# Optimization experiments

Hardware: AMD Instinct MI355X
Metric: run time of the kernel (lower is better)

Reference implementation:

```python
import jax, jax.numpy as jnp
import numpy as np

S, B, D = 2048, 2, 1024
H, DH = 16, 64
DFF = 4096
E, K = 4, 2
SCALE = 1.0 / (DH ** 0.5)


def _ln(x, g, b, eps):
    m = jnp.mean(x, axis=-1, keepdims=True)
    v = jnp.mean((x - m) ** 2, axis=-1, keepdims=True)
    return (x - m) * jax.lax.rsqrt(v + eps) * g + b


def setup_inputs() -> dict:
    key = jax.random.key(0)
    ks = jax.random.split(key, 12)
    s = lambda k, shape, fan: jax.random.normal(k, shape, jnp.float32) * (fan ** -0.5)
    return {
        "hidden_states": jax.random.normal(ks[0], (S, B, D), jnp.float32),
        "ln_in_g": jnp.ones((D,), jnp.float32), "ln_in_b": jnp.zeros((D,), jnp.float32),
        "Wq": s(ks[1], (D, H * DH), D),
        "Wkv": s(ks[2], (D, 2 * H * DH), D),
        "Wo": s(ks[3], (H * DH, D), H * DH),
        "ln_attn_g": jnp.ones((D,), jnp.float32), "ln_attn_b": jnp.zeros((D,), jnp.float32),
        "ln_post_g": jnp.ones((D,), jnp.float32), "ln_post_b": jnp.zeros((D,), jnp.float32),
        "Wg": s(ks[4], (D, E), D),
        "W1": s(ks[5], (E, D, DFF), D), "b1": jnp.zeros((E, DFF), jnp.float32),
        "W2": s(ks[6], (E, DFF, D), DFF), "b2": jnp.zeros((E, D), jnp.float32),
    }


def reference(hidden_states, ln_in_g, ln_in_b, Wq, Wkv, Wo, ln_attn_g, ln_attn_b,
              ln_post_g, ln_post_b, Wg, W1, b1, W2, b2):
    # --- input layernorm (eps=1e-6) ---
    h = _ln(hidden_states, ln_in_g, ln_in_b, 1e-6)  # [S,B,D]

    # --- MultiHeadAttn2 (post-lnorm, no mask, no mems) ---
    q = (h @ Wq).reshape(S, B, H, DH)
    k, v = jnp.split((h @ Wkv).reshape(S, B, H, 2 * DH), 2, axis=-1)
    score = jnp.einsum('ibnd,jbnd->ijbn', q, k) * SCALE      # [S,S,B,H]
    prob = jax.nn.softmax(score, axis=1)
    attn_vec = jnp.einsum('ijbn,jbnd->ibnd', prob, v).reshape(S, B, H * DH)
    attn_out = attn_vec @ Wo
    attention_output = _ln(h + attn_out, ln_attn_g, ln_attn_b, 1e-5)

    # --- residual + post-attention layernorm (eps=1e-6) ---
    layernorm_input = hidden_states + attention_output
    x = _ln(layernorm_input, ln_post_g, ln_post_b, 1e-6)

    # --- top-k MoE (E=4, k=2, no token dropping) ---
    xt = x.reshape(-1, D)                                     # [T,D]
    probs = jax.nn.softmax(xt @ Wg, axis=-1)                  # [T,E]
    topv, topi = jax.lax.top_k(probs, K)                      # [T,K]
    gates = topv / jnp.sum(topv, axis=-1, keepdims=True)
    cw = jnp.zeros_like(probs)
    for kk in range(K):  # small fixed K
        cw = cw + gates[:, kk:kk + 1] * jax.nn.one_hot(topi[:, kk], E, dtype=probs.dtype)
    hmid = jax.nn.gelu(jnp.einsum('td,edf->tef', xt, W1) + b1, approximate=False)
    y = jnp.einsum('tef,efd->ted', hmid, W2) + b2             # [T,E,D]
    moe_out = jnp.einsum('te,ted->td', cw, y).reshape(S, B, D)

    # load-balancing aux loss: E * sum(mean_probs * top1_fraction)
    me = jnp.mean(probs, axis=0)
    ce = jnp.mean(jax.nn.one_hot(topi[:, 0], E, dtype=probs.dtype), axis=0)
    moe_loss = E * jnp.sum(me * ce)

    output = layernorm_input + moe_out
    return output, moe_loss
```

## Files before the change

kernel.cpp:

```cpp
#include <hip/hip_runtime.h>
#include <cmath>

#define S_   2048
#define B_   2
#define D_   1024
#define H_   16
#define DH_  64
#define DFF_ 4096
#define E_   4
#define T_   4096
#define SCALE_ 0.125f

typedef __attribute__((ext_vector_type(8))) short short8;
typedef __attribute__((ext_vector_type(4))) float f32x4;
typedef __attribute__((ext_vector_type(4))) unsigned short u16x4;
typedef __attribute__((ext_vector_type(4))) unsigned int u32x4;

static __device__ __forceinline__ unsigned short f2bf(float f) {
  union { float f; unsigned int u; } v; v.f = f;
  unsigned int r = v.u + 0x7FFFu + ((v.u >> 16) & 1u);
  return (unsigned short)(r >> 16);
}

static __device__ __forceinline__ float bf2f(unsigned short u) {
  union { unsigned int u; float f; } v; v.u = (unsigned int)u << 16;
  return v.f;
}

static __device__ __forceinline__ f32x4 mfma16(short8 a, short8 b, f32x4 c) {
  return __builtin_amdgcn_mfma_f32_16x16x32_bf16(a, b, c, 0, 0, 0);
}

static __device__ __forceinline__ void gll16(const unsigned short* g, unsigned short* l) {
  __builtin_amdgcn_global_load_lds(
      (const __attribute__((address_space(1))) void*)g,
      (__attribute__((address_space(3))) void*)l, 16, 0, 0);
}

static __device__ __forceinline__ float gelu_f(float vv) {
  float u = 0.7978845608f * (vv + 0.044715f * vv * vv * vv);
  u = fminf(fmaxf(u, -9.0f), 9.0f);
  float e2 = __expf(2.0f * u);
  return vv * e2 * (1.0f / (e2 + 1.0f));
}

__global__ void transpose_cvt(const float* __restrict__ in, unsigned short* __restrict__ out,
                              int R, int C) {
  __shared__ float t[64][33];
  size_t boff = (size_t)blockIdx.z * R * C;
  in += boff; out += boff;
  int c0 = blockIdx.x * 32, r0 = blockIdx.y * 64;
  for (int i = threadIdx.y; i < 64; i += 8)
    t[i][threadIdx.x] = in[(size_t)(r0 + i) * C + c0 + threadIdx.x];
  __syncthreads();
  for (int i = threadIdx.y; i < 32; i += 8) {
    float v0 = t[2 * threadIdx.x][i], v1 = t[2 * threadIdx.x + 1][i];
    unsigned int pk = (unsigned int)f2bf(v0) | ((unsigned int)f2bf(v1) << 16);
    *(unsigned int*)(&out[(size_t)(c0 + i) * R + r0 + 2 * threadIdx.x]) = pk;
  }
}

__global__ void transpose_cvt_split(const float* __restrict__ in,
    unsigned short* __restrict__ outh, unsigned short* __restrict__ outl, int R, int C) {
  __shared__ float t[64][33];
  int c0 = blockIdx.x * 32, r0 = blockIdx.y * 64;
  for (int i = threadIdx.y; i < 64; i += 8)
    t[i][threadIdx.x] = in[(size_t)(r0 + i) * C + c0 + threadIdx.x];
  __syncthreads();
  for (int i = threadIdx.y; i < 32; i += 8) {
    float v0 = t[2 * threadIdx.x][i], v1 = t[2 * threadIdx.x + 1][i];
    unsigned short h0 = f2bf(v0), h1 = f2bf(v1);
    unsigned int hp = (unsigned int)h0 | ((unsigned int)h1 << 16);
    unsigned int lp = (unsigned int)f2bf(v0 - bf2f(h0)) |
                      ((unsigned int)f2bf(v1 - bf2f(h1)) << 16);
    size_t o = (size_t)(c0 + i) * R + r0 + 2 * threadIdx.x;
    *(unsigned int*)(&outh[o]) = hp;
    *(unsigned int*)(&outl[o]) = lp;
  }
}

__global__ __launch_bounds__(256) void v_transpose(
    const unsigned short* __restrict__ kvh, const unsigned short* __restrict__ kvl,
    unsigned short* __restrict__ vTh, unsigned short* __restrict__ vTl) {
  __shared__ unsigned short th[64][72], tl[64][72];
  int j0 = blockIdx.x * 64;
  int bh = blockIdx.y;
  int b = bh & 1, n = bh >> 1;
  int tid = threadIdx.x;
  int jr = tid >> 3, dc = (tid & 7) * 8;
  for (int it = 0; it < 2; ++it) {
    int jj = it * 32 + jr;
    size_t src = ((size_t)((j0 + jj) * 2 + b)) * 2048 + n * 128 + 64 + dc;
    *(short8*)(&th[jj][dc]) = *(const short8*)(kvh + src);
    *(short8*)(&tl[jj][dc]) = *(const short8*)(kvl + src);
  }
  __syncthreads();
  int dr = tid >> 3, jc = (tid & 7) * 8;
  for (int it = 0; it < 2; ++it) {
    int d = it * 32 + dr;
    short8 oh, ol;
    for (int u = 0; u < 8; ++u) { oh[u] = th[jc + u][d]; ol[u] = tl[jc + u][d]; }
    size_t dst = ((size_t)((b * 16 + n) * 64 + d)) * 2048 + j0 + jc;
    *(short8*)(vTh + dst) = oh;
    *(short8*)(vTl + dst) = ol;
  }
}

static __device__ __forceinline__ void block_reduce2(float& s, float& s2, float* sh) {
  __syncthreads();
  for (int off = 32; off; off >>= 1) { s += __shfl_down(s, off); s2 += __shfl_down(s2, off); }
  int w = threadIdx.x >> 6;
  if ((threadIdx.x & 63) == 0) { sh[w * 2] = s; sh[w * 2 + 1] = s2; }
  __syncthreads();
  s = sh[0] + sh[2] + sh[4] + sh[6];
  s2 = sh[1] + sh[3] + sh[5] + sh[7];
}

__global__ __launch_bounds__(256) void ln_in_kernel(const float* __restrict__ hid,
    const float* __restrict__ g, const float* __restrict__ b,
    float* __restrict__ h, unsigned short* __restrict__ hbh, unsigned short* __restrict__ hbl) {
  __shared__ float sh[8];
  int t = blockIdx.x, tid = threadIdx.x;
  size_t ro = (size_t)t * D_;
  f32x4 v = ((const f32x4*)(hid + ro))[tid];
  float s = v[0] + v[1] + v[2] + v[3];
  float s2 = v[0]*v[0] + v[1]*v[1] + v[2]*v[2] + v[3]*v[3];
  block_reduce2(s, s2, sh);
  float mean = s * (1.0f / D_);
  float var = s2 * (1.0f / D_) - mean * mean;
  float rstd = rsqrtf(var + 1e-6f);
  f32x4 gv = ((const f32x4*)g)[tid], bv = ((const f32x4*)b)[tid];
  f32x4 y; u16x4 yh, yl;
  for (int c = 0; c < 4; ++c) {
    float z = (v[c] - mean) * rstd * gv[c] + bv[c];
    y[c] = z; yh[c] = f2bf(z); yl[c] = f2bf(z - bf2f(yh[c]));
  }
  ((f32x4*)(h + ro))[tid] = y;
  ((u16x4*)(hbh + ro))[tid] = yh;
  ((u16x4*)(hbl + ro))[tid] = yl;
}

__global__ __launch_bounds__(256) void ln_fused_kernel(
    const float* __restrict__ hid, const float* __restrict__ h, const float* __restrict__ ao,
    const float* __restrict__ ga, const float* __restrict__ ba,
    const float* __restrict__ gp, const float* __restrict__ bp,
    float* __restrict__ out, float* __restrict__ x, unsigned short* __restrict__ xb) {
  __shared__ float sh[8];
  int t = blockIdx.x, tid = threadIdx.x;
  size_t ro = (size_t)t * D_;
  f32x4 hv = ((const f32x4*)(h + ro))[tid];
  f32x4 av = ((const f32x4*)(ao + ro))[tid];
  f32x4 a = hv + av;
  float s = a[0] + a[1] + a[2] + a[3];
  float s2 = a[0]*a[0] + a[1]*a[1] + a[2]*a[2] + a[3]*a[3];
  block_reduce2(s, s2, sh);
  float mean = s * (1.0f / D_);
  float var = s2 * (1.0f / D_) - mean * mean;
  float rstd = rsqrtf(var + 1e-5f);
  f32x4 lg = ((const f32x4*)ga)[tid], lb = ((const f32x4*)ba)[tid];
  f32x4 hidv = ((const f32x4*)(hid + ro))[tid];
  f32x4 li;
  for (int c = 0; c < 4; ++c) li[c] = hidv[c] + (a[c] - mean) * rstd * lg[c] + lb[c];
  ((f32x4*)(out + ro))[tid] = li;
  float s3 = li[0] + li[1] + li[2] + li[3];
  float s4 = li[0]*li[0] + li[1]*li[1] + li[2]*li[2] + li[3]*li[3];
  block_reduce2(s3, s4, sh);
  float mean2 = s3 * (1.0f / D_);
  float var2 = s4 * (1.0f / D_) - mean2 * mean2;
  float rstd2 = rsqrtf(var2 + 1e-6f);
  f32x4 g2 = ((const f32x4*)gp)[tid], b2v = ((const f32x4*)bp)[tid];
  f32x4 xv; u16x4 xbv;
  for (int c = 0; c < 4; ++c) { float z = (li[c] - mean2) * rstd2 * g2[c] + b2v[c]; xv[c] = z; xbv[c] = f2bf(z); }
  ((f32x4*)(x + ro))[tid] = xv;
  ((u16x4*)(xb + ro))[tid] = xbv;
}

__global__ __launch_bounds__(256) void qkv_gemm(
    const unsigned short* __restrict__ Ah, const unsigned short* __restrict__ Al,
    const unsigned short* __restrict__ WqTh, const unsigned short* __restrict__ WqTl,
    const unsigned short* __restrict__ WkvTh, const unsigned short* __restrict__ WkvTl,
    unsigned short* __restrict__ qh, unsigned short* __restrict__ ql,
    unsigned short* __restrict__ kvh, unsigned short* __restrict__ kvl) {
  const int K = 1024;
  int m0 = blockIdx.y * 128, n0g = blockIdx.x * 128;
  const unsigned short *Bh, *Bl;
  unsigned short *Ch, *Cl;
  int NC, n0;
  if (n0g < 1024) { Bh = WqTh; Bl = WqTl; Ch = qh; Cl = ql; NC = 1024; n0 = n0g; }
  else { Bh = WkvTh; Bl = WkvTl; Ch = kvh; Cl = kvl; NC = 2048; n0 = n0g - 1024; }
  __shared__ unsigned short pool2[16384];
  unsigned short* Ash = pool2;
  unsigned short* Asl = pool2 + 4096;
  unsigned short* Bsh = pool2 + 8192;
  unsigned short* Bsl = pool2 + 12288;
  int tid = threadIdx.x;
  int lane = tid & 63, w = tid >> 6;
  int quad = lane >> 4, l15 = lane & 15;
  int wm = (w >> 1) * 64, wn = (w & 1) * 64;
  f32x4 acc[4][4];
  for (int i = 0; i < 4; ++i) for (int j = 0; j < 4; ++j) acc[i][j] = 0;
  int rs0 = w * 32 + (lane >> 2), rs1 = rs0 + 16;
  int cofs = (lane & 3) * 8;
  const unsigned short* gah0 = Ah + (size_t)(m0 + rs0) * K + cofs;
  const unsigned short* gah1 = Ah + (size_t)(m0 + rs1) * K + cofs;
  const unsigned short* gal0 = Al + (size_t)(m0 + rs0) * K + cofs;
  const unsigned short* gal1 = Al + (size_t)(m0 + rs1) * K + cofs;
  const unsigned short* gbh0 = Bh + (size_t)(n0 + rs0) * K + cofs;
  const unsigned short* gbh1 = Bh + (size_t)(n0 + rs1) * K + cofs;
  const unsigned short* gbl0 = Bl + (size_t)(n0 + rs0) * K + cofs;
  const unsigned short* gbl1 = Bl + (size_t)(n0 + rs1) * K + cofs;
  unsigned short* lA0 = &Ash[(w * 2 + 0) * 512];
  unsigned short* lA1 = &Ash[(w * 2 + 1) * 512];
  unsigned short* lAl0 = &Asl[(w * 2 + 0) * 512];
  unsigned short* lAl1 = &Asl[(w * 2 + 1) * 512];
  unsigned short* lB0 = &Bsh[(w * 2 + 0) * 512];
  unsigned short* lB1 = &Bsh[(w * 2 + 1) * 512];
  unsigned short* lBl0 = &Bsl[(w * 2 + 0) * 512];
  unsigned short* lBl1 = &Bsl[(w * 2 + 1) * 512];
  for (int k0 = 0; k0 < K; k0 += 32) {
    __syncthreads();
    gll16(gah0 + k0, lA0); gll16(gah1 + k0, lA1);
    gll16(gal0 + k0, lAl0); gll16(gal1 + k0, lAl1);
    gll16(gbh0 + k0, lB0); gll16(gbh1 + k0, lB1);
    gll16(gbl0 + k0, lBl0); gll16(gbl1 + k0, lBl1);
    __syncthreads();
    short8 afh[4], afl[4], bfh[4], bfl[4];
    for (int i = 0; i < 4; ++i) {
      int o = (wm + i * 16 + l15) * 32 + quad * 8;
      afh[i] = *(const short8*)(&Ash[o]);
      afl[i] = *(const short8*)(&Asl[o]);
    }
    for (int j = 0; j < 4; ++j) {
      int o = (wn + j * 16 + l15) * 32 + quad * 8;
      bfh[j] = *(const short8*)(&Bsh[o]);
      bfl[j] = *(const short8*)(&Bsl[o]);
    }
    for (int i = 0; i < 4; ++i)
      for (int j = 0; j < 4; ++j) {
        f32x4 a = acc[i][j];
        a = mfma16(afh[i], bfl[j], a);
        a = mfma16(afl[i], bfh[j], a);
        a = mfma16(afh[i], bfh[j], a);
        acc[i][j] = a;
      }
  }
  __syncthreads();
  unsigned short* eph = &pool2[w * 1152];
  unsigned short* epl = &pool2[4608 + w * 1152];
  int row16 = lane >> 3, chunk = lane & 7;
  for (int i = 0; i < 4; ++i) {
    for (int j = 0; j < 4; ++j) {
      f32x4 a = acc[i][j];
      int lo = j * 16 + l15;
      for (int r = 0; r < 4; ++r) {
        unsigned short hb = f2bf(a[r]);
        eph[(quad * 4 + r) * 72 + lo] = hb;
        epl[(quad * 4 + r) * 72 + lo] = f2bf(a[r] - bf2f(hb));
      }
    }
    for (int it = 0; it < 2; ++it) {
      int rr = it * 8 + row16;
      size_t go = (size_t)(m0 + wm + i * 16 + rr) * NC + n0 + wn + chunk * 8;
      *(u32x4*)(&Ch[go]) = *(const u32x4*)(&eph[rr * 72 + chunk * 8]);
      *(u32x4*)(&Cl[go]) = *(const u32x4*)(&epl[rr * 72 + chunk * 8]);
    }
    __syncthreads();
  }
}

template<int MT>
__global__ __launch_bounds__(256) void gemm3f(
    const unsigned short* __restrict__ Ah, const unsigned short* __restrict__ Al,
    const unsigned short* __restrict__ Bh, const unsigned short* __restrict__ Bl,
    float* __restrict__ Cf, int N, int K) {
  int m0 = blockIdx.y * MT, n0 = blockIdx.x * 128;
  __shared__ unsigned short pool3[MT * 64 + 8192];
  unsigned short* Ash = pool3;
  unsigned short* Asl = pool3 + MT * 32;
  unsigned short* Bsh = pool3 + MT * 64;
  unsigned short* Bsl = pool3 + MT * 64 + 4096;
  int tid = threadIdx.x;
  int lane = tid & 63, w = tid >> 6;
  int quad = lane >> 4, l15 = lane & 15;
  int wm = (w >> 1) * (MT / 2), wn = (w & 1) * 64;
  constexpr int MI = MT / 32;
  f32x4 acc[MI][4];
  for (int i = 0; i < MI; ++i) for (int j = 0; j < 4; ++j) acc[i][j] = 0;
  constexpr int AI = MT / 64;
  int cofs = (lane & 3) * 8;
  const unsigned short* gah[AI]; const unsigned short* gal[AI];
  unsigned short *lAh[AI], *lAl[AI];
  for (int is = 0; is < AI; ++is) {
    int rs = w * (MT / 4) + is * 16 + (lane >> 2);
    gah[is] = Ah + (size_t)(m0 + rs) * K + cofs;
    gal[is] = Al + (size_t)(m0 + rs) * K + cofs;
    lAh[is] = &Ash[(w * AI + is) * 512];
    lAl[is] = &Asl[(w * AI + is) * 512];
  }
  int rsB0 = w * 32 + (lane >> 2), rsB1 = rsB0 + 16;
  const unsigned short* gbh0 = Bh + (size_t)(n0 + rsB0) * K + cofs;
  const unsigned short* gbh1 = Bh + (size_t)(n0 + rsB1) * K + cofs;
  const unsigned short* gbl0 = Bl + (size_t)(n0 + rsB0) * K + cofs;
  const unsigned short* gbl1 = Bl + (size_t)(n0 + rsB1) * K + cofs;
  unsigned short* lB0 = &Bsh[(w * 2 + 0) * 512];
  unsigned short* lB1 = &Bsh[(w * 2 + 1) * 512];
  unsigned short* lBl0 = &Bsl[(w * 2 + 0) * 512];
  unsigned short* lBl1 = &Bsl[(w * 2 + 1) * 512];
  for (int k0 = 0; k0 < K; k0 += 32) {
    __syncthreads();
    for (int is = 0; is < AI; ++is) { gll16(gah[is] + k0, lAh[is]); gll16(gal[is] + k0, lAl[is]); }
    gll16(gbh0 + k0, lB0); gll16(gbh1 + k0, lB1);
    gll16(gbl0 + k0, lBl0); gll16(gbl1 + k0, lBl1);
    __syncthreads();
    short8 afh[MI], afl[MI], bfh[4], bfl[4];
    for (int i = 0; i < MI; ++i) {
      int o = (wm + i * 16 + l15) * 32 + quad * 8;
      afh[i] = *(const short8*)(&Ash[o]);
      afl[i] = *(const short8*)(&Asl[o]);
    }
    for (int j = 0; j < 4; ++j) {
      int o = (wn + j * 16 + l15) * 32 + quad * 8;
      bfh[j] = *(const short8*)(&Bsh[o]);
      bfl[j] = *(const short8*)(&Bsl[o]);
    }
    for (int i = 0; i < MI; ++i)
      for (int j = 0; j < 4; ++j) {
        f32x4 a = acc[i][j];
        a = mfma16(afh[i], bfl[j], a);
        a = mfma16(afl[i], bfh[j], a);
        a = mfma16(afh[i], bfh[j], a);
        acc[i][j] = a;
      }
  }
  __syncthreads();
  float* epf = (float*)(pool3 + w * 2176);
  for (int i = 0; i < MI; ++i) {
    for (int j = 0; j < 4; ++j) {
      f32x4 a = acc[i][j];
      for (int r = 0; r < 4; ++r) epf[(quad * 4 + r) * 68 + j * 16 + l15] = a[r];
    }
    for (int it = 0; it < 4; ++it) {
      int rr = (lane >> 4) + it * 4;
      int ch = lane & 15;
      *(f32x4*)(&Cf[(size_t)(m0 + wm + i * 16 + rr) * N + n0 + wn + ch * 4]) =
          *(const f32x4*)(&epf[rr * 68 + ch * 4]);
    }
    __syncthreads();
  }
}

__global__ __launch_bounds__(256) void moe_up(
    const unsigned short* __restrict__ A, const unsigned short* __restrict__ W1T,
    unsigned short* __restrict__ hmid, int N, int K,
    const int* __restrict__ cnt, const int* __restrict__ offs,
    const int* __restrict__ list, const float* __restrict__ b1) {
  int e = blockIdx.y >> 5, mt = blockIdx.y & 31;
  int M = cnt[e];
  int m0 = mt * 128, n0 = blockIdx.x * 128;
  if (M == 0 || m0 >= M) return;
  const unsigned short* Bt = W1T + (size_t)e * DFF_ * D_;
  const int* liste = list + e * T_;
  const float* bias = b1 + (size_t)e * DFF_;
  size_t obase = (size_t)offs[e];
  __shared__ unsigned short pool[16384];
  unsigned short* As0 = pool;
  unsigned short* Bs0 = pool + 4096;
  unsigned short* As1 = pool + 8192;
  unsigned short* Bs1 = pool + 12288;
  int tid = threadIdx.x;
  int lane = tid & 63, w = tid >> 6;
  int quad = lane >> 4, l15 = lane & 15;
  int wm = (w >> 1) * 64, wn = (w & 1) * 64;
  f32x4 acc[4][4];
  for (int i = 0; i < 4; ++i) for (int j = 0; j < 4; ++j) acc[i][j] = 0;
  int rs0 = w * 32 + (lane >> 2), rs1 = rs0 + 16;
  int cofs = (lane & 3) * 8;
  const unsigned short* ga0 = A + (size_t)liste[min(m0 + rs0, M - 1)] * K + cofs;
  const unsigned short* ga1 = A + (size_t)liste[min(m0 + rs1, M - 1)] * K + cofs;
  const unsigned short* gb0 = Bt + (size_t)(n0 + rs0) * K + cofs;
  const unsigned short* gb1 = Bt + (size_t)(n0 + rs1) * K + cofs;
  int so0 = (w * 2 + 0) * 512, so1 = (w * 2 + 1) * 512;
  auto stage = [&](unsigned short* Ab, unsigned short* Bb, int k) {
    gll16(ga0 + k, Ab + so0); gll16(ga1 + k, Ab + so1);
    gll16(gb0 + k, Bb + so0); gll16(gb1 + k, Bb + so1);
  };
  auto compute = [&](const unsigned short* Ab, const unsigned short* Bb) {
    short8 af[4], bfr[4];
    for (int i = 0; i < 4; ++i) af[i] = *(const short8*)(&Ab[(wm + i * 16 + l15) * 32 + quad * 8]);
    for (int j = 0; j < 4; ++j) bfr[j] = *(const short8*)(&Bb[(wn + j * 16 + l15) * 32 + quad * 8]);
    for (int i = 0; i < 4; ++i)
      for (int j = 0; j < 4; ++j)
        acc[i][j] = mfma16(af[i], bfr[j], acc[i][j]);
  };
  stage(As0, Bs0, 0);
  __syncthreads();
  for (int k0 = 0; k0 < K; k0 += 64) {
    stage(As1, Bs1, k0 + 32);
    compute(As0, Bs0);
    __syncthreads();
    if (k0 + 64 < K) stage(As0, Bs0, k0 + 64);
    compute(As1, Bs1);
    __syncthreads();
  }
  unsigned short* ep = &pool[w * 1152];
  int row16 = lane >> 3, chunk = lane & 7;
  for (int i = 0; i < 4; ++i) {
    for (int j = 0; j < 4; ++j) {
      f32x4 a = acc[i][j];
      int colg = n0 + wn + j * 16 + l15;
      float bv = bias[colg];
      for (int r = 0; r < 4; ++r)
        ep[(quad * 4 + r) * 72 + j * 16 + l15] = f2bf(gelu_f(a[r] + bv));
    }
    for (int it = 0; it < 2; ++it) {
      int rr = it * 8 + row16;
      int rowg = m0 + wm + i * 16 + rr;
      if (rowg < M)
        *(u32x4*)(&hmid[(obase + rowg) * DFF_ + n0 + wn + chunk * 8]) =
            *(const u32x4*)(&ep[rr * 72 + chunk * 8]);
    }
  }
}

__global__ __launch_bounds__(256) void moe_down(
    const unsigned short* __restrict__ hmid, const unsigned short* __restrict__ W2T,
    int N, int K,
    const int* __restrict__ cnt, const int* __restrict__ offs,
    const int* __restrict__ list, const float* __restrict__ gatev,
    const float* __restrict__ b2, float* __restrict__ accum) {
  int e = blockIdx.y >> 6, mt = blockIdx.y & 63;
  int M = cnt[e];
  int m0 = mt * 64, n0 = blockIdx.x * 128;
  if (M == 0 || m0 >= M) return;
  const unsigned short* A = hmid + (size_t)offs[e] * DFF_;
  const unsigned short* Bt = W2T + (size_t)e * D_ * DFF_;
  const int* liste = list + e * T_;
  const float* gv = gatev + e * T_;
  const float* bias = b2 + (size_t)e * D_;
  __shared__ unsigned short As0[2048], Bs0[4096], As1[2048], Bs1[4096];
  int tid = threadIdx.x;
  int lane = tid & 63, w = tid >> 6;
  int quad = lane >> 4, l15 = lane & 15;
  int wm = (w >> 1) * 32, wn = (w & 1) * 64;
  f32x4 acc[2][4];
  for (int i = 0; i < 2; ++i) for (int j = 0; j < 4; ++j) acc[i][j] = 0;
  int rsA = w * 16 + (lane >> 2);
  int rsB0 = w * 32 + (lane >> 2), rsB1 = rsB0 + 16;
  int cofs = (lane & 3) * 8;
  const unsigned short* ga = A + (size_t)min(m0 + rsA, M - 1) * K + cofs;
  const unsigned short* gb0 = Bt + (size_t)(n0 + rsB0) * K + cofs;
  const unsigned short* gb1 = Bt + (size_t)(n0 + rsB1) * K + cofs;
  int soA = w * 512;
  int so0 = (w * 2 + 0) * 512, so1 = (w * 2 + 1) * 512;
  auto stage = [&](unsigned short* Ab, unsigned short* Bb, int k) {
    gll16(ga + k, Ab + soA);
    gll16(gb0 + k, Bb + so0); gll16(gb1 + k, Bb + so1);
  };
  auto compute = [&](const unsigned short* Ab, const unsigned short* Bb) {
    short8 af[2], bfr[4];
    for (int i = 0; i < 2; ++i) af[i] = *(const short8*)(&Ab[(wm + i * 16 + l15) * 32 + quad * 8]);
    for (int j = 0; j < 4; ++j) bfr[j] = *(const short8*)(&Bb[(wn + j * 16 + l15) * 32 + quad * 8]);
    for (int i = 0; i < 2; ++i)
      for (int j = 0; j < 4; ++j)
        acc[i][j] = mfma16(af[i], bfr[j], acc[i][j]);
  };
  stage(As0, Bs0, 0);
  __syncthreads();
  for (int k0 = 0; k0 < K; k0 += 64) {
    stage(As1, Bs1, k0 + 32);
    compute(As0, Bs0);
    __syncthreads();
    if (k0 + 64 < K) stage(As0, Bs0, k0 + 64);
    compute(As1, Bs1);
    __syncthreads();
  }
  for (int i = 0; i < 2; ++i) for (int j = 0; j < 4; ++j) {
    int row = m0 + wm + i * 16 + quad * 4;
    int col = n0 + wn + j * 16 + l15;
    f32x4 a = acc[i][j];
    float bv = bias[col];
    for (int r = 0; r < 4; ++r) if (row + r < M) {
      int tt = liste[row + r];
      float gg = gv[row + r];
      atomicAdd(&accum[(size_t)tt * D_ + col], gg * (a[r] + bv));
    }
  }
}

__global__ __launch_bounds__(256, 2) void attn_kernel(
    const unsigned short* __restrict__ qh, const unsigned short* __restrict__ ql,
    const unsigned short* __restrict__ kvh, const unsigned short* __restrict__ kvl,
    const unsigned short* __restrict__ vTh, const unsigned short* __restrict__ vTl,
    unsigned short* __restrict__ avh, unsigned short* __restrict__ avl) {
  int bh = blockIdx.x;
  int itile = blockIdx.y;
  int b = bh & 1, n = bh >> 1;
  __shared__ unsigned short Kh[2][4096], Kl[2][4096], Vh[2][4096], Vl[2][4096];
  __shared__ unsigned short Ps[4][1152];
  int tid = threadIdx.x;
  int w = tid >> 6, lane = tid & 63, quad = lane >> 4, l15 = lane & 15;
  int i_base = itile * 64 + w * 16;
  short8 qfh[2], qfl[2];
  {
    size_t qo = ((size_t)((i_base + l15) * B_ + b)) * 1024 + n * 64;
    qfh[0] = *(const short8*)(qh + qo + quad * 8);
    qfh[1] = *(const short8*)(qh + qo + 32 + quad * 8);
    qfl[0] = *(const short8*)(ql + qo + quad * 8);
    qfl[1] = *(const short8*)(ql + qo + 32 + quad * 8);
  }
  float m_i[4], l_i[4];
  f32x4 o[4];
  for (int r = 0; r < 4; ++r) { m_i[r] = -1e30f; l_i[r] = 0.0f; }
  for (int d = 0; d < 4; ++d) o[d] = 0;
  int jk = tid >> 3;
  int ck = (tid & 7) ^ (jk & 7);
  size_t kS = ((size_t)(jk * 2 + b)) * 2048 + (size_t)n * 128 + ck * 8;
  size_t vS = ((size_t)((b * 16 + n) * 64 + jk)) * 2048 + ck * 8;
  int ldst = tid * 8;
  unsigned short* psw = &Ps[w][0];
  gll16(kvh + kS, &Kh[0][ldst]);           gll16(kvh + kS + 131072, &Kh[0][2048 + ldst]);
  gll16(kvl + kS, &Kl[0][ldst]);           gll16(kvl + kS + 131072, &Kl[0][2048 + ldst]);
  gll16(vTh + vS, &Vh[0][ldst]);           gll16(vTh + vS + 65536, &Vh[0][2048 + ldst]);
  gll16(vTl + vS, &Vl[0][ldst]);           gll16(vTl + vS + 65536, &Vl[0][2048 + ldst]);
  __syncthreads();
  for (int jt = 0; jt < 32; ++jt) {
    int cur = jt & 1;
    if (jt < 31) {
      int nb = cur ^ 1;
      size_t ks2 = kS + (size_t)(jt + 1) * 262144;
      size_t vs2 = vS + (size_t)(jt + 1) * 64;
      gll16(kvh + ks2, &Kh[nb][ldst]);     gll16(kvh + ks2 + 131072, &Kh[nb][2048 + ldst]);
      gll16(kvl + ks2, &Kl[nb][ldst]);     gll16(kvl + ks2 + 131072, &Kl[nb][2048 + ldst]);
      gll16(vTh + vs2, &Vh[nb][ldst]);     gll16(vTh + vs2 + 65536, &Vh[nb][2048 + ldst]);
      gll16(vTl + vs2, &Vl[nb][ldst]);     gll16(vTl + vs2 + 65536, &Vl[nb][2048 + ldst]);
    }
    f32x4 sac[4];
    __builtin_amdgcn_s_setprio(1);
    for (int t4 = 0; t4 < 4; ++t4) {
      int j = t4 * 16 + l15;
      int base = j * 64;
      int c0 = (quad ^ (j & 7)) << 3;
      int c1 = ((quad | 4) ^ (j & 7)) << 3;
      short8 kh0 = *(const short8*)(&Kh[cur][base + c0]);
      short8 kh1 = *(const short8*)(&Kh[cur][base + c1]);
      short8 kl0 = *(const short8*)(&Kl[cur][base + c0]);
      short8 kl1 = *(const short8*)(&Kl[cur][base + c1]);
      f32x4 a = 0;
      a = mfma16(qfh[0], kl0, a);
      a = mfma16(qfh[1], kl1, a);
      a = mfma16(qfl[0], kh0, a);
      a = mfma16(qfl[1], kh1, a);
      a = mfma16(qfh[0], kh0, a);
      a = mfma16(qfh[1], kh1, a);
      sac[t4] = a;
    }
    __builtin_amdgcn_s_setprio(0);
    float p[4][4];
    float alpha[4];
    for (int r = 0; r < 4; ++r) {
      float m1 = fmaxf(fmaxf(sac[0][r], sac[1][r]), fmaxf(sac[2][r], sac[3][r])) * SCALE_;
      for (int off = 1; off < 16; off <<= 1) m1 = fmaxf(m1, __shfl_xor(m1, off, 16));
      float mnew = fmaxf(m_i[r], m1);
      alpha[r] = __expf(m_i[r] - mnew);
      m_i[r] = mnew;
      float rs = 0.f;
      for (int t4 = 0; t4 < 4; ++t4) {
        float pp = __expf(sac[t4][r] * SCALE_ - mnew);
        p[t4][r] = pp; rs += pp;
      }
      for (int off = 1; off < 16; off <<= 1) rs += __shfl_xor(rs, off, 16);
      l_i[r] = l_i[r] * alpha[r] + rs;
    }
    for (int d = 0; d < 4; ++d) for (int r = 0; r < 4; ++r) o[d][r] *= alpha[r];
    for (int t4 = 0; t4 < 4; ++t4) for (int r = 0; r < 4; ++r)
      psw[(quad * 4 + r) * 72 + t4 * 16 + l15] = f2bf(p[t4][r]);
    __builtin_amdgcn_s_setprio(1);
    for (int dblk = 0; dblk < 4; ++dblk) {
      f32x4 a = o[dblk];
      int d = dblk * 16 + l15;
      int vb = d * 64;
      for (int ks = 0; ks < 2; ++ks) {
        short8 pfh = *(const short8*)(&psw[l15 * 72 + ks * 32 + quad * 8]);
        int ch = ((ks * 4 + quad) ^ (d & 7)) << 3;
        short8 vfh = *(const short8*)(&Vh[cur][vb + ch]);
        short8 vfl = *(const short8*)(&Vl[cur][vb + ch]);
        a = mfma16(pfh, vfl, a);
        a = mfma16(pfh, vfh, a);
      }
      o[dblk] = a;
    }
    __builtin_amdgcn_s_setprio(0);
    __syncthreads();
  }
  {
    int row16 = lane >> 3, chunk = lane & 7;
    for (int d = 0; d < 4; ++d) for (int r = 0; r < 4; ++r) {
      float val = o[d][r] / l_i[r];
      psw[(quad * 4 + r) * 72 + d * 16 + l15] = f2bf(val);
    }
    for (int it = 0; it < 2; ++it) {
      int rr = it * 8 + row16;
      size_t go = ((size_t)((i_base + rr) * B_ + b)) * 1024 + n * 64 + chunk * 8;
      *(u32x4*)(&avh[go]) = *(const u32x4*)(&psw[rr * 72 + chunk * 8]);
    }
    __syncthreads();
    for (int d = 0; d < 4; ++d) for (int r = 0; r < 4; ++r) {
      float val = o[d][r] / l_i[r];
      unsigned short hb = f2bf(val);
      psw[(quad * 4 + r) * 72 + d * 16 + l15] = f2bf(val - bf2f(hb));
    }
    for (int it = 0; it < 2; ++it) {
      int rr = it * 8 + row16;
      size_t go = ((size_t)((i_base + rr) * B_ + b)) * 1024 + n * 64 + chunk * 8;
      *(u32x4*)(&avl[go]) = *(const u32x4*)(&psw[rr * 72 + chunk * 8]);
    }
  }
}

__global__ __launch_bounds__(256) void gate_kernel(const float* __restrict__ x,
    const float* __restrict__ Wg, int* __restrict__ cnt,
    float* __restrict__ me_sum, float* __restrict__ ce_sum,
    int* __restrict__ list, float* __restrict__ gatev) {
  __shared__ float sl[64][4];
  int w = threadIdx.x >> 6, lane = threadIdx.x & 63;
  int tbase = blockIdx.x * 64;
  for (int k = 0; k < 16; ++k) {
    int t = tbase + w * 16 + k;
    f32x4 acc = 0;
    const float* xr = x + (size_t)t * D_;
    for (int j = 0; j < 16; ++j) {
      int d = j * 64 + lane;
      float xd = xr[d];
      f32x4 wg = ((const f32x4*)Wg)[d];
      acc += xd * wg;
    }
    for (int c = 0; c < 4; ++c) {
      float vv = acc[c];
      for (int off = 32; off; off >>= 1) vv += __shfl_down(vv, off);
      if (lane == 0) sl[w * 16 + k][c] = vv;
    }
  }
  __syncthreads();
  if (w == 0) {
    int t = tbase + lane;
    float p[4];
    float mx = fmaxf(fmaxf(sl[lane][0], sl[lane][1]), fmaxf(sl[lane][2], sl[lane][3]));
    float sum = 0.f;
    for (int e = 0; e < 4; ++e) { p[e] = expf(sl[lane][e] - mx); sum += p[e]; }
    float inv = 1.0f / sum;
    for (int e = 0; e < 4; ++e) p[e] *= inv;
    int i0 = 0;
    for (int e = 1; e < 4; ++e) if (p[e] > p[i0]) i0 = e;
    int i1 = (i0 == 0) ? 1 : 0;
    for (int e = 0; e < 4; ++e) if (e != i0 && p[e] > p[i1]) i1 = e;
    float g0 = p[i0] / (p[i0] + p[i1]);
    float g1 = p[i1] / (p[i0] + p[i1]);
    for (int e = 0; e < 4; ++e) {
      float vv = p[e];
      for (int off = 32; off; off >>= 1) vv += __shfl_down(vv, off);
      if (lane == 0) atomicAdd(&me_sum[e], vv);
    }
    unsigned long long lbm = (1ull << lane) - 1;
    for (int e = 0; e < 4; ++e) {
      unsigned long long m0 = __ballot(i0 == e);
      int tot = __popcll(m0);
      int base = 0;
      if (lane == e && tot > 0) {
        base = atomicAdd(&cnt[e], tot);
        atomicAdd(&ce_sum[e], (float)tot);
      }
      base = __shfl(base, e);
      if (i0 == e) {
        int pos = base + __popcll(m0 & lbm);
        list[e * T_ + pos] = t;
        gatev[e * T_ + pos] = g0;
      }
      unsigned long long m1 = __ballot(i1 == e);
      int tot1 = __popcll(m1);
      int base1 = 0;
      if (lane == e && tot1 > 0) base1 = atomicAdd(&cnt[e], tot1);
      base1 = __shfl(base1, e);
      if (i1 == e) {
        int pos = base1 + __popcll(m1 & lbm);
        list[e * T_ + pos] = t;
        gatev[e * T_ + pos] = g1;
      }
    }
  }
}

__global__ void loss_offs_kernel(const float* __restrict__ me, const float* __restrict__ ce,
                                 const int* __restrict__ cnt, int* __restrict__ offs,
                                 float* __restrict__ out) {
  if (threadIdx.x == 0) {
    float l = 0.f;
    for (int e = 0; e < E_; ++e) l += (me[e] * (1.0f / T_)) * (ce[e] * (1.0f / T_));
    out[0] = (float)E_ * l;
    int o = 0;
    for (int e = 0; e < E_; ++e) { offs[e] = o; o += cnt[e]; }
  }
}

extern "C" void kernel_launch(void* const* d_in, const int* in_sizes, int n_in,
                              void* d_out, int out_size, void* d_ws, size_t ws_size,
                              hipStream_t stream) {
  const float* hid       = (const float*)d_in[0];
  const float* ln_in_g   = (const float*)d_in[1];
  const float* ln_in_b   = (const float*)d_in[2];
  const float* Wq        = (const float*)d_in[3];
  const float* Wkv       = (const float*)d_in[4];
  const float* Wo        = (const float*)d_in[5];
  const float* ln_attn_g = (const float*)d_in[6];
  const float* ln_attn_b = (const float*)d_in[7];
  const float* ln_post_g = (const float*)d_in[8];
  const float* ln_post_b = (const float*)d_in[9];
  const float* Wg        = (const float*)d_in[10];
  const float* W1        = (const float*)d_in[11];
  const float* b1        = (const float*)d_in[12];
  const float* W2        = (const float*)d_in[13];
  const float* b2        = (const float*)d_in[14];
  float* out = (float*)d_out;

  char* p = (char*)d_ws;
  size_t off = 0;
  auto alloc = [&](size_t bytes) -> void* {
    void* r = p + off; off += (bytes + 255) & ~(size_t)255; return r;
  };
  float* h        = (float*)alloc((size_t)T_ * D_ * 4);
  float* x        = (float*)alloc((size_t)T_ * D_ * 4);
  unsigned short* hmid_all = (unsigned short*)h;
  unsigned short* qh = (unsigned short*)alloc((size_t)T_ * 1024 * 2);
  unsigned short* ql = (unsigned short*)alloc((size_t)T_ * 1024 * 2);
  float* attn_out = (float*)qh;
  unsigned short* hbh = (unsigned short*)alloc((size_t)T_ * D_ * 2);
  unsigned short* hbl = (unsigned short*)alloc((size_t)T_ * D_ * 2);
  unsigned short* vTh = hbh;
  unsigned short* vTl = hbl;
  unsigned short* xb  = (unsigned short*)alloc((size_t)T_ * D_ * 2);
  unsigned short* kvh = (unsigned short*)alloc((size_t)T_ * 2048 * 2);
  unsigned short* kvl = (unsigned short*)alloc((size_t)T_ * 2048 * 2);
  unsigned short* W1T = kvh;
  unsigned short* avh = (unsigned short*)alloc((size_t)T_ * 1024 * 2);
  unsigned short* avl = (unsigned short*)alloc((size_t)T_ * 1024 * 2);
  unsigned short* W2T = avh;
  unsigned short* WqTh  = (unsigned short*)alloc((size_t)1024 * 1024 * 2);
  unsigned short* WqTl  = (unsigned short*)alloc((size_t)1024 * 1024 * 2);
  unsigned short* WkvTh = (unsigned short*)alloc((size_t)2048 * 1024 * 2);
  unsigned short* WkvTl = (unsigned short*)alloc((size_t)2048 * 1024 * 2);
  unsigned short* WoTh  = (unsigned short*)alloc((size_t)1024 * 1024 * 2);
  unsigned short* WoTl  = (unsigned short*)alloc((size_t)1024 * 1024 * 2);
  void* ghdr = alloc(256);
  int* cnt = (int*)ghdr;
  float* me_sum = (float*)ghdr + 4;
  float* ce_sum = (float*)ghdr + 8;
  int* offs = (int*)ghdr + 12;
  int* list = (int*)alloc((size_t)E_ * T_ * 4);
  float* gatev = (float*)alloc((size_t)E_ * T_ * 4);

  hipMemsetAsync(ghdr, 0, 64, stream);

  dim3 tb(32, 8);
  transpose_cvt_split<<<dim3(32, 16), tb, 0, stream>>>(Wq, WqTh, WqTl, 1024, 1024);
  transpose_cvt_split<<<dim3(64, 16), tb, 0, stream>>>(Wkv, WkvTh, WkvTl, 1024, 2048);
  transpose_cvt_split<<<dim3(32, 16), tb, 0, stream>>>(Wo, WoTh, WoTl, 1024, 1024);

  ln_in_kernel<<<T_, 256, 0, stream>>>(hid, ln_in_g, ln_in_b, h, hbh, hbl);

  qkv_gemm<<<dim3(24, 32), 256, 0, stream>>>(hbh, hbl, WqTh, WqTl, WkvTh, WkvTl,
      qh, ql, kvh, kvl);

  v_transpose<<<dim3(32, 32), 256, 0, stream>>>(kvh, kvl, vTh, vTl);

  attn_kernel<<<dim3(32, 32), 256, 0, stream>>>(qh, ql, kvh, kvl, vTh, vTl, avh, avl);

  gemm3f<64><<<dim3(8, 64), 256, 0, stream>>>(avh, avl, WoTh, WoTl, attn_out, 1024, 1024);

  ln_fused_kernel<<<T_, 256, 0, stream>>>(hid, h, attn_out, ln_attn_g, ln_attn_b,
      ln_post_g, ln_post_b, out, x, xb);

  gate_kernel<<<T_ / 64, 256, 0, stream>>>(x, Wg, cnt, me_sum, ce_sum, list, gatev);
  loss_offs_kernel<<<1, 64, 0, stream>>>(me_sum, ce_sum, cnt, offs, out + (size_t)T_ * D_);

  transpose_cvt<<<dim3(128, 16, 4), tb, 0, stream>>>(W1, W1T, 1024, 4096);
  transpose_cvt<<<dim3(32, 64, 4), tb, 0, stream>>>(W2, W2T, 4096, 1024);

  moe_up<<<dim3(32, 128), 256, 0, stream>>>(xb, W1T, hmid_all, DFF_, 1024,
      cnt, offs, list, b1);
  moe_down<<<dim3(8, 256), 256, 0, stream>>>(hmid_all, W2T, D_, DFF_,
      cnt, offs, list, gatev, b2, out);
}
```

Baseline: 894.8 us.

## Swizzle LDS tiles in MoE GEMMs and enlarge down-proj M tile

Adds an XOR swizzle to the 16-byte column chunks in the global-to-LDS loads of moe_up and moe_down, and applies the matching swizzle on the MFMA fragment reads, to reduce LDS bank conflicts. moe_down's M tile grows from 64 to 128 rows, giving 4x4 accumulators per wave, and its grid shrinks to match. This raises operand reuse per block but uses more registers and LDS, and leaves fewer blocks to fill the device.

```diff
diff --git a/kernel.cpp b/kernel.cpp
--- a/kernel.cpp
+++ b/kernel.cpp
@@ -374,20 +374,23 @@
   f32x4 acc[4][4];
   for (int i = 0; i < 4; ++i) for (int j = 0; j < 4; ++j) acc[i][j] = 0;
   int rs0 = w * 32 + (lane >> 2), rs1 = rs0 + 16;
-  int cofs = (lane & 3) * 8;
-  const unsigned short* ga0 = A + (size_t)liste[min(m0 + rs0, M - 1)] * K + cofs;
-  const unsigned short* ga1 = A + (size_t)liste[min(m0 + rs1, M - 1)] * K + cofs;
-  const unsigned short* gb0 = Bt + (size_t)(n0 + rs0) * K + cofs;
-  const unsigned short* gb1 = Bt + (size_t)(n0 + rs1) * K + cofs;
+  int sw = ((lane & 3) ^ ((lane >> 3) & 3)) * 8;
+  const unsigned short* ga0 = A + (size_t)liste[min(m0 + rs0, M - 1)] * K + sw;
+  const unsigned short* ga1 = A + (size_t)liste[min(m0 + rs1, M - 1)] * K + sw;
+  const unsigned short* gb0 = Bt + (size_t)(n0 + rs0) * K + sw;
+  const unsigned short* gb1 = Bt + (size_t)(n0 + rs1) * K + sw;
   int so0 = (w * 2 + 0) * 512, so1 = (w * 2 + 1) * 512;
+  int sq = (l15 >> 1) & 3;
   auto stage = [&](unsigned short* Ab, unsigned short* Bb, int k) {
     gll16(ga0 + k, Ab + so0); gll16(ga1 + k, Ab + so1);
     gll16(gb0 + k, Bb + so0); gll16(gb1 + k, Bb + so1);
   };
   auto compute = [&](const unsigned short* Ab, const unsigned short* Bb) {
     short8 af[4], bfr[4];
-    for (int i = 0; i < 4; ++i) af[i] = *(const short8*)(&Ab[(wm + i * 16 + l15) * 32 + quad * 8]);
-    for (int j = 0; j < 4; ++j) bfr[j] = *(const short8*)(&Bb[(wn + j * 16 + l15) * 32 + quad * 8]);
+    for (int i = 0; i < 4; ++i)
+      af[i] = *(const short8*)(&Ab[(wm + i * 16 + l15) * 32 + (quad ^ sq) * 8]);
+    for (int j = 0; j < 4; ++j)
+      bfr[j] = *(const short8*)(&Bb[(wn + j * 16 + l15) * 32 + (quad ^ sq) * 8]);
     for (int i = 0; i < 4; ++i)
       for (int j = 0; j < 4; ++j)
         acc[i][j] = mfma16(af[i], bfr[j], acc[i][j]);
@@ -428,39 +431,45 @@
     const int* __restrict__ cnt, const int* __restrict__ offs,
     const int* __restrict__ list, const float* __restrict__ gatev,
     const float* __restrict__ b2, float* __restrict__ accum) {
-  int e = blockIdx.y >> 6, mt = blockIdx.y & 63;
+  int e = blockIdx.y >> 5, mt = blockIdx.y & 31;
   int M = cnt[e];
-  int m0 = mt * 64, n0 = blockIdx.x * 128;
+  int m0 = mt * 128, n0 = blockIdx.x * 128;
   if (M == 0 || m0 >= M) return;
   const unsigned short* A = hmid + (size_t)offs[e] * DFF_;
   const unsigned short* Bt = W2T + (size_t)e * D_ * DFF_;
   const int* liste = list + e * T_;
   const float* gv = gatev + e * T_;
   const float* bias = b2 + (size_t)e * D_;
-  __shared__ unsigned short As0[2048], Bs0[4096], As1[2048], Bs1[4096];
+  __shared__ unsigned short pool[16384];
+  unsigned short* As0 = pool;
+  unsigned short* Bs0 = pool + 4096;
+  unsigned short* As1 = pool + 8192;
+  unsigned short* Bs1 = pool + 12288;
   int tid = threadIdx.x;
   int lane = tid & 63, w = tid >> 6;
   int quad = lane >> 4, l15 = lane & 15;
-  int wm = (w >> 1) * 32, wn = (w & 1) * 64;
-  f32x4 acc[2][4];
-  for (int i = 0; i < 2; ++i) for (int j = 0; j < 4; ++j) acc[i][j] = 0;
-  int rsA = w * 16 + (lane >> 2);
-  int rsB0 = w * 32 + (lane >> 2), rsB1 = rsB0 + 16;
-  int cofs = (lane & 3) * 8;
-  const unsigned short* ga = A + (size_t)min(m0 + rsA, M - 1) * K + cofs;
-  const unsigned short* gb0 = Bt + (size_t)(n0 + rsB0) * K + cofs;
-  const unsigned short* gb1 = Bt + (size_t)(n0 + rsB1) * K + cofs;
-  int soA = w * 512;
+  int wm = (w >> 1) * 64, wn = (w & 1) * 64;
+  f32x4 acc[4][4];
+  for (int i = 0; i < 4; ++i) for (int j = 0; j < 4; ++j) acc[i][j] = 0;
+  int rs0 = w * 32 + (lane >> 2), rs1 = rs0 + 16;
+  int sw = ((lane & 3) ^ ((lane >> 3) & 3)) * 8;
+  const unsigned short* ga0 = A + (size_t)min(m0 + rs0, M - 1) * K + sw;
+  const unsigned short* ga1 = A + (size_t)min(m0 + rs1, M - 1) * K + sw;
+  const unsigned short* gb0 = Bt + (size_t)(n0 + rs0) * K + sw;
+  const unsigned short* gb1 = Bt + (size_t)(n0 + rs1) * K + sw;
   int so0 = (w * 2 + 0) * 512, so1 = (w * 2 + 1) * 512;
+  int sq = (l15 >> 1) & 3;
   auto stage = [&](unsigned short* Ab, unsigned short* Bb, int k) {
-    gll16(ga + k, Ab + soA);
+    gll16(ga0 + k, Ab + so0); gll16(ga1 + k, Ab + so1);
     gll16(gb0 + k, Bb + so0); gll16(gb1 + k, Bb + so1);
   };
   auto compute = [&](const unsigned short* Ab, const unsigned short* Bb) {
-    short8 af[2], bfr[4];
-    for (int i = 0; i < 2; ++i) af[i] = *(const short8*)(&Ab[(wm + i * 16 + l15) * 32 + quad * 8]);
-    for (int j = 0; j < 4; ++j) bfr[j] = *(const short8*)(&Bb[(wn + j * 16 + l15) * 32 + quad * 8]);
-    for (int i = 0; i < 2; ++i)
+    short8 af[4], bfr[4];
+    for (int i = 0; i < 4; ++i)
+      af[i] = *(const short8*)(&Ab[(wm + i * 16 + l15) * 32 + (quad ^ sq) * 8]);
+    for (int j = 0; j < 4; ++j)
+      bfr[j] = *(const short8*)(&Bb[(wn + j * 16 + l15) * 32 + (quad ^ sq) * 8]);
+    for (int i = 0; i < 4; ++i)
       for (int j = 0; j < 4; ++j)
         acc[i][j] = mfma16(af[i], bfr[j], acc[i][j]);
   };
@@ -474,7 +483,7 @@
     compute(As1, Bs1);
     __syncthreads();
   }
-  for (int i = 0; i < 2; ++i) for (int j = 0; j < 4; ++j) {
+  for (int i = 0; i < 4; ++i) for (int j = 0; j < 4; ++j) {
     int row = m0 + wm + i * 16 + quad * 4;
     int col = n0 + wn + j * 16 + l15;
     f32x4 a = acc[i][j];
@@ -786,6 +795,6 @@
 
   moe_up<<<dim3(32, 128), 256, 0, stream>>>(xb, W1T, hmid_all, DFF_, 1024,
       cnt, offs, list, b1);
-  moe_down<<<dim3(8, 256), 256, 0, stream>>>(hmid_all, W2T, D_, DFF_,
+  moe_down<<<dim3(8, 128), 256, 0, stream>>>(hmid_all, W2T, D_, DFF_,
       cnt, offs, list, gatev, b2, out);
 }
```

Result: no change. 880.0 us (-1.7%).
